# Optimization experiments

Measured on AMD Instinct MI355X. Metric: run time of the kernel, lower is better.

Reference implementation:

```python
import jax, jax.numpy as jnp
import numpy as np

EMBED_DIM = 192
KERNEL_MUL = 2.0
KERNEL_NUM = 5


def setup_inputs() -> dict:
    key = jax.random.key(0)
    k1, k2, k3 = jax.random.split(key, 3)
    x = jax.random.normal(k1, (8192, EMBED_DIM), dtype=jnp.float32)
    label = jax.random.randint(k2, (8192,), 0, 1000, dtype=jnp.int32)
    genre_label = jax.random.randint(k3, (8192,), 0, 8, dtype=jnp.int32)
    return {"x": x, "label": label, "genre_label": genre_label}


def reference(x, label, genre_label):
    # even rows -> source, odd rows -> target (label/genre_label unused by the loss)
    source = x[::2].reshape(-1, EMBED_DIM)
    target = x[1::2].reshape(-1, EMBED_DIM)
    total = jnp.concatenate([source, target], axis=0)  # [N, D]
    n = total.shape[0]
    n_samples = n  # source rows + target rows

    # pairwise squared L2 via ||a||^2 + ||b||^2 - 2 a.b (avoids N x N x D buffer)
    sq = jnp.sum(total * total, axis=1)  # [N]
    L2 = sq[:, None] + sq[None, :] - 2.0 * (total @ total.T)  # [N, N]
    L2 = jnp.maximum(L2, 0.0)

    # bandwidth from detached distances (matches torch .data)
    bandwidth = jax.lax.stop_gradient(jnp.sum(L2)) / (n_samples ** 2 - n_samples)
    bandwidth = bandwidth / (KERNEL_MUL ** (KERNEL_NUM // 2))

    # multi-bandwidth RBF kernel sum
    kernels = jnp.zeros_like(L2)
    for i in range(KERNEL_NUM):
        kernels = kernels + jnp.exp(-L2 / (bandwidth * (KERNEL_MUL ** i)))

    x_n = source.shape[0]
    y_n = target.shape[0]
    xx = kernels[:x_n, :x_n]
    yy = kernels[y_n:, y_n:]
    xy = kernels[:x_n, y_n:]
    yx = kernels[y_n:, :x_n]
    loss = jnp.mean(xx + yy - xy - yx)
    return loss
```

## Files before the change

### kernel.cpp

```cpp
#include <hip/hip_runtime.h>
#include <math.h>

#define N_TOTAL 8192
#define HALF    4096
#define EMBED   192
#define BT      128
#define NT      (N_TOTAL / BT)
#define NBLK    (NT * (NT + 1) / 2)
#define KC      96
#define PADK    104

typedef short     bf16x8 __attribute__((ext_vector_type(8)));
typedef float     f32x4  __attribute__((ext_vector_type(4)));


__device__ __forceinline__ unsigned pack2_bf16(float a, float b) {
    unsigned ua = __float_as_uint(a), ub = __float_as_uint(b);
    unsigned ha = (ua + 0x7FFFu + ((ua >> 16) & 1u)) >> 16;
    unsigned hb = (ub + 0x7FFFu + ((ub >> 16) & 1u)) >> 16;
    return ha | (hb << 16);
}

__global__ __launch_bounds__(256) void row_stats(
    const float* __restrict__ x, float* __restrict__ sq,
    float* __restrict__ colsum, double* __restrict__ sumsq_all) {
    __shared__ float  ls_col[EMBED];
    __shared__ double ls_sq[8];
    int t = threadIdx.x, w = t >> 5, lane = t & 31;
    if (t < EMBED) ls_col[t] = 0.f;
    __syncthreads();

    double wsq = 0.0;
#pragma unroll
    for (int q = 0; q < 4; ++q) {
        int r = blockIdx.x * 32 + w * 4 + q;
        const float* xr = x + (size_t)r * EMBED;
        float s = 0.f, vals[6];
#pragma unroll
        for (int m = 0; m < 6; ++m) {
            float v = xr[lane + 32 * m];
            vals[m] = v;
            s += v * v;
        }
#pragma unroll
        for (int off = 16; off; off >>= 1) s += __shfl_down(s, off, 32);
        if (lane == 0) {
            int g = (r & 1) ? (HALF + (r >> 1)) : (r >> 1);
            sq[g] = s;
            wsq += (double)s;
        }
#pragma unroll
        for (int m = 0; m < 6; ++m) atomicAdd(&ls_col[lane + 32 * m], vals[m]);
    }
    if (lane == 0) ls_sq[w] = wsq;
    __syncthreads();
    if (t < EMBED) atomicAdd(&colsum[t], ls_col[t]);
    if (t == 0) {
        double b = 0.0;
#pragma unroll
        for (int m = 0; m < 8; ++m) b += ls_sq[m];
        atomicAdd(sumsq_all, b);
    }
}

__global__ __launch_bounds__(256) void convert_bf16(
    const float* __restrict__ x, unsigned short* __restrict__ xb) {
    int u = blockIdx.x * 256 + threadIdx.x;
    int r = u / 24;
    int c = (u - r * 24) * 8;
    int g = (r & 1) ? (HALF + (r >> 1)) : (r >> 1);
    const float* src = x + (size_t)r * EMBED + c;
    float4 f0 = *(const float4*)src;
    float4 f1 = *(const float4*)(src + 4);
    uint4 o;
    o.x = pack2_bf16(f0.x, f0.y);
    o.y = pack2_bf16(f0.z, f0.w);
    o.z = pack2_bf16(f1.x, f1.y);
    o.w = pack2_bf16(f1.z, f1.w);
    *(uint4*)(xb + (size_t)g * EMBED + c) = o;
}

__global__ void finalize_bw(const float* __restrict__ colsum,
                            const double* __restrict__ sumsq_all,
                            float* __restrict__ inv_c) {
    if (threadIdx.x == 0 && blockIdx.x == 0) {
        double s2 = 0.0;
        for (int k = 0; k < EMBED; ++k) {
            double c = (double)colsum[k];
            s2 += c * c;
        }
        double n = (double)N_TOTAL;
        double sumL2 = 2.0 * n * (*sumsq_all) - 2.0 * s2;
        double bw = sumL2 / (n * n - n) / 4.0;
        *inv_c = (float)(1.0 / (16.0 * bw));
    }
}

__global__ __launch_bounds__(256, 3) void mmd_mfma(
    const unsigned short* __restrict__ xb, const float* __restrict__ sq,
    const float* __restrict__ inv_c, double* __restrict__ acc_out) {
    int id = blockIdx.x, bi = 0;
    while (id >= NT - bi) { id -= NT - bi; ++bi; }
    int bj = bi + id;
    int I0 = bi * BT, J0 = bj * BT;

    __shared__ unsigned short As[BT][PADK];
    __shared__ unsigned short Bs[BT][PADK];
    __shared__ double wred[4];

    int t = threadIdx.x, lane = t & 63, wid = t >> 6;
    int wy = (wid >> 1) * 64, wx = (wid & 1) * 64;
    int lo = lane & 15, kg = lane >> 4;

    f32x4 acc[4][4];
#pragma unroll
    for (int i = 0; i < 4; ++i)
#pragma unroll
        for (int j = 0; j < 4; ++j) acc[i][j] = (f32x4)(0.f);

    for (int kc0 = 0; kc0 < EMBED; kc0 += KC) {
        for (int s = t; s < 2 * BT * (KC / 8); s += 256) {
            int tile = s / (BT * (KC / 8));
            int rem  = s - tile * (BT * (KC / 8));
            int r    = rem / (KC / 8);
            int c    = (rem - r * (KC / 8)) * 8;
            int g    = (tile ? J0 : I0) + r;
            uint4 v  = *(const uint4*)(xb + (size_t)g * EMBED + kc0 + c);
            unsigned short* dst = tile ? &Bs[r][c] : &As[r][c];
            *(uint4*)dst = v;
        }
        __syncthreads();
#pragma unroll
        for (int kk = 0; kk < KC; kk += 32) {
            bf16x8 a[4], b[4];
#pragma unroll
            for (int i = 0; i < 4; ++i) a[i] = *(const bf16x8*)&As[wy + i * 16 + lo][kk + kg * 8];
#pragma unroll
            for (int j = 0; j < 4; ++j) b[j] = *(const bf16x8*)&Bs[wx + j * 16 + lo][kk + kg * 8];
#pragma unroll
            for (int i = 0; i < 4; ++i)
#pragma unroll
                for (int j = 0; j < 4; ++j)
                    acc[i][j] = __builtin_amdgcn_mfma_f32_16x16x32_bf16(a[i], b[j], acc[i][j], 0, 0, 0);
        }
        __syncthreads();
    }

    const float cc = *inv_c;
    int gi0 = I0 + wy + kg * 4;
    int gj0 = J0 + wx + lo;
    float sqi[4][4], sqj[4];
#pragma unroll
    for (int i = 0; i < 4; ++i)
#pragma unroll
        for (int r = 0; r < 4; ++r) sqi[i][r] = sq[gi0 + i * 16 + r];
#pragma unroll
    for (int j = 0; j < 4; ++j) sqj[j] = sq[gj0 + j * 16];

    float sgn  = ((bi < NT / 2) == (bj < NT / 2)) ? 1.f : -1.f;
    bool  diag = (bi == bj);
    float tsum = 0.f;
#pragma unroll
    for (int i = 0; i < 4; ++i)
#pragma unroll
        for (int j = 0; j < 4; ++j)
#pragma unroll
            for (int r = 0; r < 4; ++r) {
                float L2 = sqi[i][r] + sqj[j] - 2.f * acc[i][j][r];
                L2 = fmaxf(L2, 0.f);
                float u   = __expf(-L2 * cc);
                float u2  = u * u;
                float u4  = u2 * u2;
                float u8  = u4 * u4;
                float u16 = u8 * u8;
                float w = 2.f;
                if (diag) {
                    int gi = gi0 + i * 16 + r, gj = gj0 + j * 16;
                    w = (gi < gj) ? 2.f : ((gi == gj) ? 1.f : 0.f);
                }
                tsum += w * (u + u2 + u4 + u8 + u16);
            }
    tsum *= sgn;

#pragma unroll
    for (int off = 32; off; off >>= 1) tsum += __shfl_down(tsum, off, 64);
    if (lane == 0) wred[wid] = (double)tsum;
    __syncthreads();
    if (t == 0) atomicAdd(acc_out, wred[0] + wred[1] + wred[2] + wred[3]);
}

__global__ void finalize_loss(const double* __restrict__ acc, float* __restrict__ out) {
    if (threadIdx.x == 0 && blockIdx.x == 0)
        out[0] = (float)(*acc / ((double)HALF * (double)HALF));
}

extern "C" void kernel_launch(void* const* d_in, const int* in_sizes, int n_in,
                              void* d_out, int out_size, void* d_ws, size_t ws_size,
                              hipStream_t stream) {
    const float* x = (const float*)d_in[0];

    double*         d_sumsq  = (double*)d_ws;
    double*         d_acc    = (double*)d_ws + 1;
    float*          d_colsum = (float*)((char*)d_ws + 16);
    float*          d_invc   = (float*)((char*)d_ws + 784);
    float*          d_sq     = (float*)((char*)d_ws + 800);
    unsigned short* d_xb     = (unsigned short*)((char*)d_ws + 33568);

    hipMemsetAsync(d_ws, 0, 800, stream);

    row_stats<<<N_TOTAL / 32, 256, 0, stream>>>(x, d_sq, d_colsum, d_sumsq);
    convert_bf16<<<(N_TOTAL * (EMBED / 8)) / 256, 256, 0, stream>>>(x, d_xb);
    finalize_bw<<<1, 1, 0, stream>>>(d_colsum, d_sumsq, d_invc);
    mmd_mfma<<<NBLK, 256, 0, stream>>>(d_xb, d_sq, d_invc, d_acc);
    finalize_loss<<<1, 1, 0, stream>>>(d_acc, (float*)d_out);
}
```

Measured before the change: 132.1 us.

## Fuse prep kernels, load MFMA operands directly from global, split diagonal epilogue

Merges row statistics and bf16 conversion into one prep kernel that reads x once, and parallelises the bandwidth finalize across 256 threads. The MFMA kernel drops its LDS staging and barriers and loads bf16x8 fragments straight from global memory (relying on L1/L2 reuse). The epilogue is split so off-diagonal tiles skip the per-element triangle weight logic. Direct global loads give up LDS sharing between waves and can add L2 traffic and latency.

```diff
diff --git a/kernel.cpp b/kernel.cpp
--- a/kernel.cpp
+++ b/kernel.cpp
@@ -7,11 +7,9 @@
 #define BT      128
 #define NT      (N_TOTAL / BT)
 #define NBLK    (NT * (NT + 1) / 2)
-#define KC      96
-#define PADK    104
-
-typedef short     bf16x8 __attribute__((ext_vector_type(8)));
-typedef float     f32x4  __attribute__((ext_vector_type(4)));
+
+typedef short bf16x8 __attribute__((ext_vector_type(8)));
+typedef float f32x4  __attribute__((ext_vector_type(4)));
 
 
 __device__ __forceinline__ unsigned pack2_bf16(float a, float b) {
@@ -21,75 +19,72 @@
     return ha | (hb << 16);
 }
 
-__global__ __launch_bounds__(256) void row_stats(
-    const float* __restrict__ x, float* __restrict__ sq,
-    float* __restrict__ colsum, double* __restrict__ sumsq_all) {
+__global__ __launch_bounds__(256) void prep(
+    const float* __restrict__ x, unsigned short* __restrict__ xb,
+    float* __restrict__ sq, float* __restrict__ colsum,
+    double* __restrict__ sumsq_all) {
     __shared__ float  ls_col[EMBED];
-    __shared__ double ls_sq[8];
-    int t = threadIdx.x, w = t >> 5, lane = t & 31;
+    __shared__ double ls_sq[4];
+    int t = threadIdx.x;
     if (t < EMBED) ls_col[t] = 0.f;
     __syncthreads();
 
-    double wsq = 0.0;
-#pragma unroll
-    for (int q = 0; q < 4; ++q) {
-        int r = blockIdx.x * 32 + w * 4 + q;
-        const float* xr = x + (size_t)r * EMBED;
-        float s = 0.f, vals[6];
-#pragma unroll
-        for (int m = 0; m < 6; ++m) {
-            float v = xr[lane + 32 * m];
-            vals[m] = v;
-            s += v * v;
-        }
-#pragma unroll
-        for (int off = 16; off; off >>= 1) s += __shfl_down(s, off, 32);
-        if (lane == 0) {
-            int g = (r & 1) ? (HALF + (r >> 1)) : (r >> 1);
-            sq[g] = s;
-            wsq += (double)s;
-        }
-#pragma unroll
-        for (int m = 0; m < 6; ++m) atomicAdd(&ls_col[lane + 32 * m], vals[m]);
-    }
-    if (lane == 0) ls_sq[w] = wsq;
+    int r   = blockIdx.x * 32 + (t >> 3);
+    int sub = t & 7;
+    int g   = (r & 1) ? (HALF + (r >> 1)) : (r >> 1);
+    const float*    src = x  + (size_t)r * EMBED;
+    unsigned short* dst = xb + (size_t)g * EMBED;
+
+    float  s = 0.f;
+    float4 v[6];
+#pragma unroll
+    for (int m = 0; m < 6; ++m) {
+        v[m] = *(const float4*)(src + (sub + 8 * m) * 4);
+        s += v[m].x * v[m].x + v[m].y * v[m].y + v[m].z * v[m].z + v[m].w * v[m].w;
+    }
+#pragma unroll
+    for (int m = 0; m < 6; ++m) {
+        uint2 o;
+        o.x = pack2_bf16(v[m].x, v[m].y);
+        o.y = pack2_bf16(v[m].z, v[m].w);
+        *(uint2*)(dst + (sub + 8 * m) * 4) = o;
+    }
+    s += __shfl_xor(s, 1, 64);
+    s += __shfl_xor(s, 2, 64);
+    s += __shfl_xor(s, 4, 64);
+    if (sub == 0) sq[g] = s;
+#pragma unroll
+    for (int m = 0; m < 6; ++m) {
+        int c = (sub + 8 * m) * 4;
+        atomicAdd(&ls_col[c + 0], v[m].x);
+        atomicAdd(&ls_col[c + 1], v[m].y);
+        atomicAdd(&ls_col[c + 2], v[m].z);
+        atomicAdd(&ls_col[c + 3], v[m].w);
+    }
+    float bs = (sub == 0) ? s : 0.f;
+    bs += __shfl_xor(bs, 8, 64);
+    bs += __shfl_xor(bs, 16, 64);
+    bs += __shfl_xor(bs, 32, 64);
+    if ((t & 63) == 0) ls_sq[t >> 6] = (double)bs;
     __syncthreads();
     if (t < EMBED) atomicAdd(&colsum[t], ls_col[t]);
+    if (t == 0) atomicAdd(sumsq_all, ls_sq[0] + ls_sq[1] + ls_sq[2] + ls_sq[3]);
+}
+
+__global__ __launch_bounds__(256) void finalize_bw(
+    const float* __restrict__ colsum, const double* __restrict__ sumsq_all,
+    float* __restrict__ inv_c) {
+    __shared__ double ws[4];
+    int t = threadIdx.x;
+    double c = (t < EMBED) ? (double)colsum[t] : 0.0;
+    double p = c * c;
+#pragma unroll
+    for (int off = 32; off; off >>= 1) p += __shfl_down(p, off, 64);
+    if ((t & 63) == 0) ws[t >> 6] = p;
+    __syncthreads();
     if (t == 0) {
-        double b = 0.0;
-#pragma unroll
-        for (int m = 0; m < 8; ++m) b += ls_sq[m];
-        atomicAdd(sumsq_all, b);
-    }
-}
-
-__global__ __launch_bounds__(256) void convert_bf16(
-    const float* __restrict__ x, unsigned short* __restrict__ xb) {
-    int u = blockIdx.x * 256 + threadIdx.x;
-    int r = u / 24;
-    int c = (u - r * 24) * 8;
-    int g = (r & 1) ? (HALF + (r >> 1)) : (r >> 1);
-    const float* src = x + (size_t)r * EMBED + c;
-    float4 f0 = *(const float4*)src;
-    float4 f1 = *(const float4*)(src + 4);
-    uint4 o;
-    o.x = pack2_bf16(f0.x, f0.y);
-    o.y = pack2_bf16(f0.z, f0.w);
-    o.z = pack2_bf16(f1.x, f1.y);
-    o.w = pack2_bf16(f1.z, f1.w);
-    *(uint4*)(xb + (size_t)g * EMBED + c) = o;
-}
-
-__global__ void finalize_bw(const float* __restrict__ colsum,
-                            const double* __restrict__ sumsq_all,
-                            float* __restrict__ inv_c) {
-    if (threadIdx.x == 0 && blockIdx.x == 0) {
-        double s2 = 0.0;
-        for (int k = 0; k < EMBED; ++k) {
-            double c = (double)colsum[k];
-            s2 += c * c;
-        }
-        double n = (double)N_TOTAL;
+        double s2 = ws[0] + ws[1] + ws[2] + ws[3];
+        double n  = (double)N_TOTAL;
         double sumL2 = 2.0 * n * (*sumsq_all) - 2.0 * s2;
         double bw = sumL2 / (n * n - n) / 4.0;
         *inv_c = (float)(1.0 / (16.0 * bw));
@@ -104,46 +99,33 @@
     int bj = bi + id;
     int I0 = bi * BT, J0 = bj * BT;
 
-    __shared__ unsigned short As[BT][PADK];
-    __shared__ unsigned short Bs[BT][PADK];
     __shared__ double wred[4];
 
     int t = threadIdx.x, lane = t & 63, wid = t >> 6;
     int wy = (wid >> 1) * 64, wx = (wid & 1) * 64;
     int lo = lane & 15, kg = lane >> 4;
 
+    const unsigned short* pA = xb + (size_t)(I0 + wy + lo) * EMBED + kg * 8;
+    const unsigned short* pB = xb + (size_t)(J0 + wx + lo) * EMBED + kg * 8;
+
     f32x4 acc[4][4];
 #pragma unroll
     for (int i = 0; i < 4; ++i)
 #pragma unroll
         for (int j = 0; j < 4; ++j) acc[i][j] = (f32x4)(0.f);
 
-    for (int kc0 = 0; kc0 < EMBED; kc0 += KC) {
-        for (int s = t; s < 2 * BT * (KC / 8); s += 256) {
-            int tile = s / (BT * (KC / 8));
-            int rem  = s - tile * (BT * (KC / 8));
-            int r    = rem / (KC / 8);
-            int c    = (rem - r * (KC / 8)) * 8;
-            int g    = (tile ? J0 : I0) + r;
-            uint4 v  = *(const uint4*)(xb + (size_t)g * EMBED + kc0 + c);
-            unsigned short* dst = tile ? &Bs[r][c] : &As[r][c];
-            *(uint4*)dst = v;
-        }
-        __syncthreads();
-#pragma unroll
-        for (int kk = 0; kk < KC; kk += 32) {
-            bf16x8 a[4], b[4];
-#pragma unroll
-            for (int i = 0; i < 4; ++i) a[i] = *(const bf16x8*)&As[wy + i * 16 + lo][kk + kg * 8];
-#pragma unroll
-            for (int j = 0; j < 4; ++j) b[j] = *(const bf16x8*)&Bs[wx + j * 16 + lo][kk + kg * 8];
-#pragma unroll
-            for (int i = 0; i < 4; ++i)
-#pragma unroll
-                for (int j = 0; j < 4; ++j)
-                    acc[i][j] = __builtin_amdgcn_mfma_f32_16x16x32_bf16(a[i], b[j], acc[i][j], 0, 0, 0);
-        }
-        __syncthreads();
+#pragma unroll
+    for (int kk = 0; kk < EMBED; kk += 32) {
+        bf16x8 a[4], b[4];
+#pragma unroll
+        for (int i = 0; i < 4; ++i) a[i] = *(const bf16x8*)(pA + i * 16 * EMBED + kk);
+#pragma unroll
+        for (int j = 0; j < 4; ++j) b[j] = *(const bf16x8*)(pB + j * 16 * EMBED + kk);
+#pragma unroll
+        for (int i = 0; i < 4; ++i)
+#pragma unroll
+            for (int j = 0; j < 4; ++j)
+                acc[i][j] = __builtin_amdgcn_mfma_f32_16x16x32_bf16(a[i], b[j], acc[i][j], 0, 0, 0);
     }
 
     const float cc = *inv_c;
@@ -158,28 +140,43 @@
     for (int j = 0; j < 4; ++j) sqj[j] = sq[gj0 + j * 16];
 
     float sgn  = ((bi < NT / 2) == (bj < NT / 2)) ? 1.f : -1.f;
-    bool  diag = (bi == bj);
     float tsum = 0.f;
-#pragma unroll
-    for (int i = 0; i < 4; ++i)
-#pragma unroll
-        for (int j = 0; j < 4; ++j)
-#pragma unroll
-            for (int r = 0; r < 4; ++r) {
-                float L2 = sqi[i][r] + sqj[j] - 2.f * acc[i][j][r];
-                L2 = fmaxf(L2, 0.f);
-                float u   = __expf(-L2 * cc);
-                float u2  = u * u;
-                float u4  = u2 * u2;
-                float u8  = u4 * u4;
-                float u16 = u8 * u8;
-                float w = 2.f;
-                if (diag) {
+    if (bi != bj) {
+#pragma unroll
+        for (int i = 0; i < 4; ++i)
+#pragma unroll
+            for (int j = 0; j < 4; ++j)
+#pragma unroll
+                for (int r = 0; r < 4; ++r) {
+                    float L2 = sqi[i][r] + sqj[j] - 2.f * acc[i][j][r];
+                    L2 = fmaxf(L2, 0.f);
+                    float u   = __expf(-L2 * cc);
+                    float u2  = u * u;
+                    float u4  = u2 * u2;
+                    float u8  = u4 * u4;
+                    float u16 = u8 * u8;
+                    tsum += (u + u2 + u4 + u8 + u16);
+                }
+        tsum *= 2.f;
+    } else {
+#pragma unroll
+        for (int i = 0; i < 4; ++i)
+#pragma unroll
+            for (int j = 0; j < 4; ++j)
+#pragma unroll
+                for (int r = 0; r < 4; ++r) {
                     int gi = gi0 + i * 16 + r, gj = gj0 + j * 16;
-                    w = (gi < gj) ? 2.f : ((gi == gj) ? 1.f : 0.f);
+                    float w = (gi < gj) ? 2.f : ((gi == gj) ? 1.f : 0.f);
+                    float L2 = sqi[i][r] + sqj[j] - 2.f * acc[i][j][r];
+                    L2 = fmaxf(L2, 0.f);
+                    float u   = __expf(-L2 * cc);
+                    float u2  = u * u;
+                    float u4  = u2 * u2;
+                    float u8  = u4 * u4;
+                    float u16 = u8 * u8;
+                    tsum += w * (u + u2 + u4 + u8 + u16);
                 }
-                tsum += w * (u + u2 + u4 + u8 + u16);
-            }
+    }
     tsum *= sgn;
 
 #pragma unroll
@@ -208,9 +205,8 @@
 
     hipMemsetAsync(d_ws, 0, 800, stream);
 
-    row_stats<<<N_TOTAL / 32, 256, 0, stream>>>(x, d_sq, d_colsum, d_sumsq);
-    convert_bf16<<<(N_TOTAL * (EMBED / 8)) / 256, 256, 0, stream>>>(x, d_xb);
-    finalize_bw<<<1, 1, 0, stream>>>(d_colsum, d_sumsq, d_invc);
+    prep<<<N_TOTAL / 32, 256, 0, stream>>>(x, d_xb, d_sq, d_colsum, d_sumsq);
+    finalize_bw<<<1, 256, 0, stream>>>(d_colsum, d_sumsq, d_invc);
     mmd_mfma<<<NBLK, 256, 0, stream>>>(d_xb, d_sq, d_invc, d_acc);
     finalize_loss<<<1, 1, 0, stream>>>(d_acc, (float*)d_out);
 }
```

After: 135.9 us. +2.8%, slower.
